# Kernel optimization log

Hardware: AMD Instinct MI355X
Metric: run time of the kernel (lower is better)

The kernel has to match this reference:

```python
import jax, jax.numpy as jnp
import numpy as np

IN_F = 4096
OUT_F = 11008
P8 = 128
P6 = 256
P4 = IN_F - P8 - P6  # 3712


def setup_inputs() -> dict:
    key = jax.random.key(0)
    k1, k2, k3, k4 = jax.random.split(key, 4)
    x = jax.random.normal(k1, (32, 8, IN_F), dtype=jnp.float32)
    W = jax.random.normal(k2, (OUT_F, IN_F), dtype=jnp.float32) * 0.02
    bias = jax.random.normal(k3, (OUT_F,), dtype=jnp.float32) * 0.01
    # channel permutation: first P4 channels -> 4-bit, next P6 -> 6-bit, last P8 -> 8-bit outliers
    reorder_index = jax.random.permutation(k4, IN_F).astype(jnp.int32)
    return {"x": x, "W": W, "bias": bias, "reorder_index": reorder_index}


def _quant(v, bits):
    # symmetric per-row quantization (per-token for acts, per-out-channel for weights)
    qmax = float(2 ** (bits - 1) - 1)
    s = jnp.max(jnp.abs(v), axis=-1, keepdims=True) / qmax
    s = jnp.where(s == 0, jnp.ones_like(s), s)
    q = jnp.round(jnp.clip(v / s, -qmax, qmax))
    return q, s


def reference(x, W, bias, reorder_index):
    bsz, q_len, F = x.shape
    xr = x.reshape(bsz * q_len, F)[:, reorder_index]  # reorder_quantize_x gather
    Wr = W[:, reorder_index]                          # reorder_quantize_w4 gather
    y = jnp.zeros((bsz * q_len, W.shape[0]), dtype=x.dtype)
    start = 0
    for bits, n in ((4, P4), (6, P6), (8, P8)):
        qa, sa = _quant(xr[:, start:start + n], bits)      # [T,n], [T,1]
        qb, sb = _quant(Wr[:, start:start + n], bits)      # [O,n], [O,1]
        # dequantized partial matmul: (qa @ qb.T) * sa * sb.T
        y = y + jnp.einsum('tn,on->to', qa, qb) * (sa * sb.T)
        start += n
    y = y + bias
    return y.reshape(bsz, q_len, -1)
```

## Files before the change

### kernel.cpp

```cpp
#include <hip/hip_runtime.h>
#include <stdint.h>

#define T_ROWS 256
#define KF 4096
#define OF 11008

typedef int   v4i __attribute__((ext_vector_type(4)));
typedef float v4f __attribute__((ext_vector_type(4)));

typedef const __attribute__((address_space(1))) uint8_t* gptr_t;
typedef __attribute__((address_space(3))) uint8_t* lptr_t;

__global__ __launch_bounds__(256) void perm_k(const int* __restrict__ idx,
                                              int* __restrict__ src_of) {
    __shared__ uint8_t g[KF];
    __shared__ int cnt[3][256];
    const int t = threadIdx.x;
    for (int i = 0; i < 16; ++i) {
        int p = t * 16 + i;
        int seg = p < 3712 ? 0 : (p < 3968 ? 1 : 2);
        g[idx[p]] = (uint8_t)seg;
    }
    __syncthreads();
    int c0 = 0, c1 = 0, c2 = 0;
    for (int i = 0; i < 16; ++i) {
        int s = g[t * 16 + i];
        c0 += (s == 0); c1 += (s == 1); c2 += (s == 2);
    }
    cnt[0][t] = c0; cnt[1][t] = c1; cnt[2][t] = c2;
    __syncthreads();
    if (t < 3) {
        int run = 0;
        for (int i = 0; i < 256; ++i) { int v = cnt[t][i]; cnt[t][i] = run; run += v; }
    }
    __syncthreads();
    int off0 = cnt[0][t], off1 = 3712 + cnt[1][t], off2 = 3968 + cnt[2][t];
    for (int i = 0; i < 16; ++i) {
        int c = t * 16 + i;
        int s = g[c];
        int d = (s == 0) ? off0++ : (s == 1) ? off1++ : off2++;
        src_of[d] = c;
    }
}

__global__ __launch_bounds__(256) void quant_k(const float* __restrict__ x,
                                               const float* __restrict__ W,
                                               const int* __restrict__ src_of,
                                               int8_t* __restrict__ qX,
                                               int8_t* __restrict__ qW,
                                               float* __restrict__ sX,
                                               float* __restrict__ sW) {
    __shared__ float rowbuf[KF];
    __shared__ float lmax[256];
    __shared__ float sm[3];
    const int b = blockIdx.x;
    const int t = threadIdx.x;
    const float* src; int8_t* qout; float* scales; int r; int nrows;
    if (b < T_ROWS) { src = x; qout = qX; scales = sX; r = b; nrows = T_ROWS; }
    else           { src = W; qout = qW; scales = sW; r = b - T_ROWS; nrows = OF; }
    const float* row = src + (size_t)r * KF;

#pragma unroll
    for (int i = 0; i < 4; ++i) {
        v4f v = *(const v4f*)(row + i * 1024 + t * 4);
        *(v4f*)&rowbuf[i * 1024 + t * 4] = v;
    }

    const int seg = t < 232 ? 0 : (t < 248 ? 1 : 2);
    const float qmax = seg == 0 ? 7.f : (seg == 1 ? 31.f : 127.f);
    int c[16];
#pragma unroll
    for (int i = 0; i < 4; ++i) {
        v4i ci = *(const v4i*)&src_of[t * 16 + i * 4];
        c[i*4+0] = ci[0]; c[i*4+1] = ci[1]; c[i*4+2] = ci[2]; c[i*4+3] = ci[3];
    }
    __syncthreads();

    float v[16];
    float mx = 0.f;
#pragma unroll
    for (int i = 0; i < 16; ++i) { v[i] = rowbuf[c[i]]; mx = fmaxf(mx, fabsf(v[i])); }
    lmax[t] = mx;
    __syncthreads();
    const int wv = t >> 6, ln = t & 63;
    if (wv == 0) {
        float m = fmaxf(fmaxf(lmax[ln], lmax[ln + 64]), lmax[ln + 128]);
        if (ln < 40) m = fmaxf(m, lmax[ln + 192]);
#pragma unroll
        for (int off = 32; off; off >>= 1) m = fmaxf(m, __shfl_xor(m, off));
        if (ln == 0) sm[0] = m;
    } else if (wv == 1) {
        float m = ln < 16 ? lmax[232 + ln] : 0.f;
#pragma unroll
        for (int off = 8; off; off >>= 1) m = fmaxf(m, __shfl_xor(m, off));
        if (ln == 0) sm[1] = m;
    } else if (wv == 2) {
        float m = ln < 8 ? lmax[248 + ln] : 0.f;
#pragma unroll
        for (int off = 4; off; off >>= 1) m = fmaxf(m, __shfl_xor(m, off));
        if (ln == 0) sm[2] = m;
    }
    __syncthreads();
    float s = sm[seg] / qmax;
    if (s == 0.f) s = 1.f;
    if (t == 0 || t == 232 || t == 248) scales[seg * nrows + r] = s;
    union { int8_t bb[16]; v4i q; } u;
#pragma unroll
    for (int i = 0; i < 16; ++i) {
        float qv = rintf(fminf(fmaxf(v[i] / s, -qmax), qmax));
        u.bb[i] = (int8_t)qv;
    }
    *(v4i*)(qout + (size_t)r * KF + t * 16) = u.q;
}

__global__ __launch_bounds__(256, 2)
void gemm_k(const int8_t* __restrict__ qX, const int8_t* __restrict__ qW,
            const float* __restrict__ sX, const float* __restrict__ sW,
            const float* __restrict__ bias, float* __restrict__ out) {
    __shared__ __align__(16) int8_t lA[3][128 * 128];
    __shared__ __align__(16) int8_t lB[3][64 * 128];

    const int bid = blockIdx.x;
    const int swz = (bid & 7) * 43 + (bid >> 3);
    const int mb = swz & 1;
    const int nb = swz >> 1;
    const int row0 = mb * 128;
    const int col0 = nb * 64;
    const int tid = threadIdx.x;
    const int lane = tid & 63;
    const int w = tid >> 6;
    const int lr = lane >> 3;
    const int lc = lane & 7;

    v4i iacc[2][4];
    v4f facc[2][4];
#pragma unroll
    for (int m = 0; m < 2; ++m)
#pragma unroll
        for (int n = 0; n < 4; ++n) {
            iacc[m][n][0]=0; iacc[m][n][1]=0; iacc[m][n][2]=0; iacc[m][n][3]=0;
            facc[m][n][0]=0.f; facc[m][n][1]=0.f; facc[m][n][2]=0.f; facc[m][n][3]=0.f;
        }

    auto stage = [&](int bf, int kstep) {
        const int k0 = kstep * 128;
        const int sc = (lc ^ lr) << 4;
#pragma unroll
        for (int j = 0; j < 4; ++j) {
            const int row = j * 32 + w * 8;
            const uint8_t* src = (const uint8_t*)qX + (size_t)(row0 + row + lr) * KF + k0 + sc;
            __builtin_amdgcn_global_load_lds((gptr_t)src, (lptr_t)&lA[bf][row * 128], 16, 0, 0);
        }
#pragma unroll
        for (int j = 0; j < 2; ++j) {
            const int row = j * 32 + w * 8;
            const uint8_t* src = (const uint8_t*)qW + (size_t)(col0 + row + lr) * KF + k0 + sc;
            __builtin_amdgcn_global_load_lds((gptr_t)src, (lptr_t)&lB[bf][row * 128], 16, 0, 0);
        }
    };

    auto flush = [&](int seg) {
#pragma unroll
        for (int m = 0; m < 2; ++m) {
            float sa[4];
#pragma unroll
            for (int rr = 0; rr < 4; ++rr)
                sa[rr] = sX[seg * T_ROWS + row0 + w * 32 + m * 16 + ((lane >> 4) << 2) + rr];
#pragma unroll
            for (int n = 0; n < 4; ++n) {
                const float sb = sW[seg * OF + col0 + n * 16 + (lane & 15)];
#pragma unroll
                for (int rr = 0; rr < 4; ++rr) {
                    facc[m][n][rr] += (float)iacc[m][n][rr] * (sa[rr] * sb);
                    iacc[m][n][rr] = 0;
                }
            }
        }
    };

    stage(0, 0);
    stage(1, 1);
    asm volatile("s_waitcnt vmcnt(6)" ::: "memory");
    __builtin_amdgcn_s_barrier();

    int cur = 0;
    for (int t = 0; t < 32; ++t) {
        if (t < 30) stage((t + 2) % 3, t + 2);
        v4i a[2][2], b2[4][2];
        const int kg = lane >> 4;
#pragma unroll
        for (int m = 0; m < 2; ++m) {
            const int row = w * 32 + m * 16 + (lane & 15);
#pragma unroll
            for (int kk = 0; kk < 2; ++kk) {
                const int ch = (kk * 4 + kg) ^ (row & 7);
                a[m][kk] = *(const v4i*)&lA[cur][row * 128 + ch * 16];
            }
        }
#pragma unroll
        for (int n = 0; n < 4; ++n) {
            const int row = n * 16 + (lane & 15);
#pragma unroll
            for (int kk = 0; kk < 2; ++kk) {
                const int ch = (kk * 4 + kg) ^ (row & 7);
                b2[n][kk] = *(const v4i*)&lB[cur][row * 128 + ch * 16];
            }
        }
        asm volatile("s_waitcnt lgkmcnt(0)" ::: "memory");
        __builtin_amdgcn_sched_barrier(0);
#pragma unroll
        for (int kk = 0; kk < 2; ++kk)
#pragma unroll
            for (int m = 0; m < 2; ++m)
#pragma unroll
                for (int n = 0; n < 4; ++n)
                    iacc[m][n] = __builtin_amdgcn_mfma_i32_16x16x64_i8(a[m][kk], b2[n][kk], iacc[m][n], 0, 0, 0);
        if (t == 28) flush(0);
        else if (t == 30) flush(1);
        if (t < 30) {
            asm volatile("s_waitcnt vmcnt(6)" ::: "memory");
            __builtin_amdgcn_s_barrier();
        } else if (t == 30) {
            asm volatile("s_waitcnt vmcnt(0)" ::: "memory");
            __builtin_amdgcn_s_barrier();
        }
        cur = (cur == 2) ? 0 : cur + 1;
    }
    flush(2);

#pragma unroll
    for (int m = 0; m < 2; ++m)
#pragma unroll
        for (int n = 0; n < 4; ++n) {
            const int colg = col0 + n * 16 + (lane & 15);
            const float bv = bias[colg];
#pragma unroll
            for (int rr = 0; rr < 4; ++rr) {
                const int rowg = row0 + w * 32 + m * 16 + ((lane >> 4) << 2) + rr;
                out[(size_t)rowg * OF + colg] = facc[m][n][rr] + bv;
            }
        }
}

extern "C" void kernel_launch(void* const* d_in, const int* in_sizes, int n_in,
                              void* d_out, int out_size, void* d_ws, size_t ws_size,
                              hipStream_t stream) {
    const float* x    = (const float*)d_in[0];
    const float* W    = (const float*)d_in[1];
    const float* bias = (const float*)d_in[2];
    const int*   ridx = (const int*)d_in[3];
    float* out = (float*)d_out;

    uint8_t* ws = (uint8_t*)d_ws;
    int8_t* qX = (int8_t*)ws;
    int8_t* qW = (int8_t*)(ws + 1048576);
    float*  sX = (float*)(ws + 46137344);
    float*  sW = (float*)(ws + 46140416);
    int* src_of = (int*)(ws + 46272512);

    perm_k<<<1, 256, 0, stream>>>(ridx, src_of);
    quant_k<<<T_ROWS + OF, 256, 0, stream>>>(x, W, src_of, qX, qW, sX, sW);
    gemm_k<<<344, 256, 0, stream>>>(qX, qW, sX, sW, bias, out);
}
```

Baseline: 79.34 us.

## Pack 4-bit weight segment as offset nibbles to cut GEMM weight traffic

Measured after the change: 83.28 us. 1.05x slower.

```diff
diff --git a/kernel.cpp b/kernel.cpp
--- a/kernel.cpp
+++ b/kernel.cpp
@@ -4,9 +4,11 @@
 #define T_ROWS 256
 #define KF 4096
 #define OF 11008
+#define WROW 2240
 
 typedef int   v4i __attribute__((ext_vector_type(4)));
 typedef float v4f __attribute__((ext_vector_type(4)));
+typedef unsigned int u32;
 
 typedef const __attribute__((address_space(1))) uint8_t* gptr_t;
 typedef __attribute__((address_space(3))) uint8_t* lptr_t;
@@ -15,6 +17,7 @@
                                               int* __restrict__ src_of) {
     __shared__ uint8_t g[KF];
     __shared__ int cnt[3][256];
+    __shared__ int exc[3][256];
     const int t = threadIdx.x;
     for (int i = 0; i < 16; ++i) {
         int p = t * 16 + i;
@@ -29,12 +32,23 @@
     }
     cnt[0][t] = c0; cnt[1][t] = c1; cnt[2][t] = c2;
     __syncthreads();
-    if (t < 3) {
+    if (t < 192) {
+        int s = t >> 6, l = t & 63;
         int run = 0;
-        for (int i = 0; i < 256; ++i) { int v = cnt[t][i]; cnt[t][i] = run; run += v; }
-    }
-    __syncthreads();
-    int off0 = cnt[0][t], off1 = 3712 + cnt[1][t], off2 = 3968 + cnt[2][t];
+        for (int j = 0; j < 4; ++j) {
+            int x = cnt[s][j * 64 + l];
+            int inc = x;
+#pragma unroll
+            for (int off = 1; off < 64; off <<= 1) {
+                int y = __shfl_up(inc, off);
+                if (l >= off) inc += y;
+            }
+            exc[s][j * 64 + l] = run + inc - x;
+            run += __shfl(inc, 63);
+        }
+    }
+    __syncthreads();
+    int off0 = exc[0][t], off1 = 3712 + exc[1][t], off2 = 3968 + exc[2][t];
     for (int i = 0; i < 16; ++i) {
         int c = t * 16 + i;
         int s = g[c];
@@ -47,23 +61,25 @@
                                                const float* __restrict__ W,
                                                const int* __restrict__ src_of,
                                                int8_t* __restrict__ qX,
-                                               int8_t* __restrict__ qW,
+                                               uint8_t* __restrict__ qWp,
                                                float* __restrict__ sX,
-                                               float* __restrict__ sW) {
+                                               float* __restrict__ sW,
+                                               int* __restrict__ S0X) {
     __shared__ float rowbuf[KF];
     __shared__ float lmax[256];
     __shared__ float sm[3];
+    __shared__ int isum[256];
     const int b = blockIdx.x;
     const int t = threadIdx.x;
-    const float* src; int8_t* qout; float* scales; int r; int nrows;
-    if (b < T_ROWS) { src = x; qout = qX; scales = sX; r = b; nrows = T_ROWS; }
-    else           { src = W; qout = qW; scales = sW; r = b - T_ROWS; nrows = OF; }
-    const float* row = src + (size_t)r * KF;
-
-#pragma unroll
-    for (int i = 0; i < 4; ++i) {
-        v4f v = *(const v4f*)(row + i * 1024 + t * 4);
-        *(v4f*)&rowbuf[i * 1024 + t * 4] = v;
+    const int w = t >> 6, lane = t & 63;
+    const bool isX = b < T_ROWS;
+    const int r = isX ? b : b - T_ROWS;
+    const float* row = (isX ? x : W) + (size_t)r * KF;
+
+#pragma unroll
+    for (int j = 0; j < 4; ++j) {
+        const uint8_t* src = (const uint8_t*)(row + j * 1024 + t * 4);
+        __builtin_amdgcn_global_load_lds((gptr_t)src, (lptr_t)&rowbuf[j * 1024 + w * 256], 16, 0, 0);
     }
 
     const int seg = t < 232 ? 0 : (t < 248 ? 1 : 2);
@@ -82,43 +98,76 @@
     for (int i = 0; i < 16; ++i) { v[i] = rowbuf[c[i]]; mx = fmaxf(mx, fabsf(v[i])); }
     lmax[t] = mx;
     __syncthreads();
-    const int wv = t >> 6, ln = t & 63;
-    if (wv == 0) {
-        float m = fmaxf(fmaxf(lmax[ln], lmax[ln + 64]), lmax[ln + 128]);
-        if (ln < 40) m = fmaxf(m, lmax[ln + 192]);
+    if (w == 0) {
+        float m = fmaxf(fmaxf(lmax[lane], lmax[lane + 64]), lmax[lane + 128]);
+        if (lane < 40) m = fmaxf(m, lmax[lane + 192]);
 #pragma unroll
         for (int off = 32; off; off >>= 1) m = fmaxf(m, __shfl_xor(m, off));
-        if (ln == 0) sm[0] = m;
-    } else if (wv == 1) {
-        float m = ln < 16 ? lmax[232 + ln] : 0.f;
+        if (lane == 0) sm[0] = m;
+    } else if (w == 1) {
+        float m = lane < 16 ? lmax[232 + lane] : 0.f;
 #pragma unroll
         for (int off = 8; off; off >>= 1) m = fmaxf(m, __shfl_xor(m, off));
-        if (ln == 0) sm[1] = m;
-    } else if (wv == 2) {
-        float m = ln < 8 ? lmax[248 + ln] : 0.f;
+        if (lane == 0) sm[1] = m;
+    } else if (w == 2) {
+        float m = lane < 8 ? lmax[248 + lane] : 0.f;
 #pragma unroll
         for (int off = 4; off; off >>= 1) m = fmaxf(m, __shfl_xor(m, off));
-        if (ln == 0) sm[2] = m;
+        if (lane == 0) sm[2] = m;
     }
     __syncthreads();
     float s = sm[seg] / qmax;
     if (s == 0.f) s = 1.f;
-    if (t == 0 || t == 232 || t == 248) scales[seg * nrows + r] = s;
-    union { int8_t bb[16]; v4i q; } u;
-#pragma unroll
-    for (int i = 0; i < 16; ++i) {
-        float qv = rintf(fminf(fmaxf(v[i] / s, -qmax), qmax));
-        u.bb[i] = (int8_t)qv;
-    }
-    *(v4i*)(qout + (size_t)r * KF + t * 16) = u.q;
+    if (t == 0 || t == 232 || t == 248)
+        (isX ? sX : sW)[seg * (isX ? T_ROWS : OF) + r] = s;
+
+    int q[16];
+#pragma unroll
+    for (int i = 0; i < 16; ++i)
+        q[i] = (int)rintf(fminf(fmaxf(v[i] / s, -qmax), qmax));
+
+    if (isX) {
+        int ss = 0;
+        union { int8_t bb[16]; v4i vv; } u;
+#pragma unroll
+        for (int i = 0; i < 16; ++i) { u.bb[i] = (int8_t)q[i]; ss += q[i]; }
+        isum[t] = (seg == 0) ? ss : 0;
+        *(v4i*)(qX + (size_t)r * KF + t * 16) = u.vv;
+        __syncthreads();
+        if (w == 0) {
+            int v2 = isum[lane] + isum[lane + 64] + isum[lane + 128] + isum[lane + 192];
+#pragma unroll
+            for (int off = 32; off; off >>= 1) v2 += __shfl_xor(v2, off);
+            if (lane == 0) S0X[r] = v2;
+        }
+    } else {
+        uint8_t* wrow = qWp + (size_t)r * WROW;
+        if (seg == 0) {
+            u32 pk[2] = {0, 0};
+#pragma unroll
+            for (int j = 0; j < 8; ++j) {
+                u32 byte = (u32)(q[2*j] + 8) | ((u32)(q[2*j+1] + 8) << 4);
+                pk[j >> 2] |= byte << ((j & 3) * 8);
+            }
+            *(u32*)(wrow + t * 8) = pk[0];
+            *(u32*)(wrow + t * 8 + 4) = pk[1];
+        } else {
+            union { int8_t bb[16]; v4i vv; } u;
+#pragma unroll
+            for (int i = 0; i < 16; ++i) u.bb[i] = (int8_t)q[i];
+            const int off = (seg == 1) ? 1856 + (t - 232) * 16 : 2112 + (t - 248) * 16;
+            *(v4i*)(wrow + off) = u.vv;
+        }
+    }
 }
 
 __global__ __launch_bounds__(256, 2)
-void gemm_k(const int8_t* __restrict__ qX, const int8_t* __restrict__ qW,
+void gemm_k(const int8_t* __restrict__ qX, const uint8_t* __restrict__ qWp,
             const float* __restrict__ sX, const float* __restrict__ sW,
+            const int* __restrict__ S0X,
             const float* __restrict__ bias, float* __restrict__ out) {
     __shared__ __align__(16) int8_t lA[3][128 * 128];
-    __shared__ __align__(16) int8_t lB[3][64 * 128];
+    __shared__ __align__(16) int8_t lB[2][64 * 128];
 
     const int bid = blockIdx.x;
     const int swz = (bid & 7) * 43 + (bid >> 3);
@@ -129,8 +178,9 @@
     const int tid = threadIdx.x;
     const int lane = tid & 63;
     const int w = tid >> 6;
-    const int lr = lane >> 3;
-    const int lc = lane & 7;
+    const int lr = lane >> 3, lc = lane & 7;
+    const int brow = tid >> 2;
+    const int bch  = tid & 3;
 
     v4i iacc[2][4];
     v4f facc[2][4];
@@ -142,59 +192,86 @@
             facc[m][n][0]=0.f; facc[m][n][1]=0.f; facc[m][n][2]=0.f; facc[m][n][3]=0.f;
         }
 
-    auto stage = [&](int bf, int kstep) {
-        const int k0 = kstep * 128;
+    auto stageA = [&](int slot, int step) {
+        const int k0 = step * 128;
         const int sc = (lc ^ lr) << 4;
 #pragma unroll
         for (int j = 0; j < 4; ++j) {
             const int row = j * 32 + w * 8;
             const uint8_t* src = (const uint8_t*)qX + (size_t)(row0 + row + lr) * KF + k0 + sc;
-            __builtin_amdgcn_global_load_lds((gptr_t)src, (lptr_t)&lA[bf][row * 128], 16, 0, 0);
-        }
-#pragma unroll
-        for (int j = 0; j < 2; ++j) {
-            const int row = j * 32 + w * 8;
-            const uint8_t* src = (const uint8_t*)qW + (size_t)(col0 + row + lr) * KF + k0 + sc;
-            __builtin_amdgcn_global_load_lds((gptr_t)src, (lptr_t)&lB[bf][row * 128], 16, 0, 0);
-        }
+            __builtin_amdgcn_global_load_lds((gptr_t)src, (lptr_t)&lA[slot][row * 128], 16, 0, 0);
+        }
+    };
+
+    auto loadB = [&](v4i (&rs)[2], int step) {
+        const uint8_t* rb = qWp + (size_t)(col0 + brow) * WROW;
+        if (step <= 28) {
+            rs[0] = *(const v4i*)(rb + step * 64 + bch * 16);
+        } else {
+            const int off = step * 128 - 1856;
+            rs[0] = *(const v4i*)(rb + off + bch * 32);
+            rs[1] = *(const v4i*)(rb + off + bch * 32 + 16);
+        }
+    };
+
+    auto writeB = [&](v4i (&rs)[2], int step) {
+        int8_t* dst = &lB[step & 1][0];
+        const int swr = brow & 7;
+        v4i w0, w1;
+        if (step <= 28) {
+#pragma unroll
+            for (int qq = 0; qq < 4; ++qq) {
+                u32 wd = ((u32)((const int*)&rs[0])[qq]);
+                u32 lo = wd & 0x0F0F0F0Fu;
+                u32 hi = (wd >> 4) & 0x0F0F0F0Fu;
+                u32 e0 = __builtin_amdgcn_perm(hi, lo, 0x05010400u);
+                u32 e1 = __builtin_amdgcn_perm(hi, lo, 0x07030602u);
+                if (qq < 2) { w0[2*qq] = (int)e0; w0[2*qq+1] = (int)e1; }
+                else        { w1[2*(qq-2)] = (int)e0; w1[2*(qq-2)+1] = (int)e1; }
+            }
+        } else {
+            w0 = rs[0]; w1 = rs[1];
+        }
+        *(v4i*)(dst + brow * 128 + ((2 * bch)     ^ swr) * 16) = w0;
+        *(v4i*)(dst + brow * 128 + ((2 * bch + 1) ^ swr) * 16) = w1;
     };
 
     auto flush = [&](int seg) {
 #pragma unroll
         for (int m = 0; m < 2; ++m) {
-            float sa[4];
-#pragma unroll
-            for (int rr = 0; rr < 4; ++rr)
-                sa[rr] = sX[seg * T_ROWS + row0 + w * 32 + m * 16 + ((lane >> 4) << 2) + rr];
+            float sa[4]; int s0[4];
+#pragma unroll
+            for (int rr = 0; rr < 4; ++rr) {
+                const int rg = row0 + w * 32 + m * 16 + ((lane >> 4) << 2) + rr;
+                sa[rr] = sX[seg * T_ROWS + rg];
+                s0[rr] = (seg == 0) ? S0X[rg] : 0;
+            }
 #pragma unroll
             for (int n = 0; n < 4; ++n) {
                 const float sb = sW[seg * OF + col0 + n * 16 + (lane & 15)];
 #pragma unroll
                 for (int rr = 0; rr < 4; ++rr) {
-                    facc[m][n][rr] += (float)iacc[m][n][rr] * (sa[rr] * sb);
+                    const int v = iacc[m][n][rr] - 8 * s0[rr];
+                    facc[m][n][rr] += (float)v * (sa[rr] * sb);
                     iacc[m][n][rr] = 0;
                 }
             }
         }
     };
 
-    stage(0, 0);
-    stage(1, 1);
-    asm volatile("s_waitcnt vmcnt(6)" ::: "memory");
-    __builtin_amdgcn_s_barrier();
-
-    int cur = 0;
-    for (int t = 0; t < 32; ++t) {
-        if (t < 30) stage((t + 2) % 3, t + 2);
-        v4i a[2][2], b2[4][2];
+    auto body = [&](int t, v4i (&rsLoad)[2], v4i (&rsWrite)[2]) {
+        __builtin_amdgcn_s_barrier();
+        v4i a[2][2], bfr[4][2];
         const int kg = lane >> 4;
+        const int8_t* pa = &lA[t % 3][0];
+        const int8_t* pb = &lB[t & 1][0];
 #pragma unroll
         for (int m = 0; m < 2; ++m) {
             const int row = w * 32 + m * 16 + (lane & 15);
 #pragma unroll
             for (int kk = 0; kk < 2; ++kk) {
                 const int ch = (kk * 4 + kg) ^ (row & 7);
-                a[m][kk] = *(const v4i*)&lA[cur][row * 128 + ch * 16];
+                a[m][kk] = *(const v4i*)(pa + row * 128 + ch * 16);
             }
         }
 #pragma unroll
@@ -203,7 +280,7 @@
 #pragma unroll
             for (int kk = 0; kk < 2; ++kk) {
                 const int ch = (kk * 4 + kg) ^ (row & 7);
-                b2[n][kk] = *(const v4i*)&lB[cur][row * 128 + ch * 16];
+                bfr[n][kk] = *(const v4i*)(pb + row * 128 + ch * 16);
             }
         }
         asm volatile("s_waitcnt lgkmcnt(0)" ::: "memory");
@@ -214,17 +291,35 @@
             for (int m = 0; m < 2; ++m)
 #pragma unroll
                 for (int n = 0; n < 4; ++n)
-                    iacc[m][n] = __builtin_amdgcn_mfma_i32_16x16x64_i8(a[m][kk], b2[n][kk], iacc[m][n], 0, 0, 0);
+                    iacc[m][n] = __builtin_amdgcn_mfma_i32_16x16x64_i8(a[m][kk], bfr[n][kk], iacc[m][n], 0, 0, 0);
         if (t == 28) flush(0);
         else if (t == 30) flush(1);
-        if (t < 30) {
-            asm volatile("s_waitcnt vmcnt(6)" ::: "memory");
-            __builtin_amdgcn_s_barrier();
-        } else if (t == 30) {
+        if (t + 2 < 32) {
+            stageA((t + 2) % 3, t + 2);
+            loadB(rsLoad, t + 2);
+            if (t + 2 <= 28) asm volatile("s_waitcnt vmcnt(5)" ::: "memory");
+            else             asm volatile("s_waitcnt vmcnt(6)" ::: "memory");
+        } else {
             asm volatile("s_waitcnt vmcnt(0)" ::: "memory");
-            __builtin_amdgcn_s_barrier();
-        }
-        cur = (cur == 2) ? 0 : cur + 1;
+        }
+        if (t + 1 < 32) {
+            writeB(rsWrite, t + 1);
+            asm volatile("s_waitcnt lgkmcnt(0)" ::: "memory");
+        }
+    };
+
+    v4i rsA_[2], rsB_[2];
+    stageA(0, 0);
+    loadB(rsA_, 0);
+    asm volatile("s_waitcnt vmcnt(0)" ::: "memory");
+    writeB(rsA_, 0);
+    stageA(1, 1);
+    loadB(rsB_, 1);
+    asm volatile("s_waitcnt lgkmcnt(0)" ::: "memory");
+
+    for (int tt = 0; tt < 32; tt += 2) {
+        body(tt,     rsA_, rsB_);
+        body(tt + 1, rsB_, rsA_);
     }
     flush(2);
 
@@ -252,13 +347,14 @@
     float* out = (float*)d_out;
 
     uint8_t* ws = (uint8_t*)d_ws;
-    int8_t* qX = (int8_t*)ws;
-    int8_t* qW = (int8_t*)(ws + 1048576);
-    float*  sX = (float*)(ws + 46137344);
-    float*  sW = (float*)(ws + 46140416);
-    int* src_of = (int*)(ws + 46272512);
+    int8_t*  qX  = (int8_t*)ws;
+    uint8_t* qWp = ws + 1048576;
+    float*   sX  = (float*)(ws + 25706496);
+    float*   sW  = (float*)(ws + 25709568);
+    int* src_of  = (int*)(ws + 25841664);
+    int* S0X     = (int*)(ws + 25858048);
 
     perm_k<<<1, 256, 0, stream>>>(ridx, src_of);
-    quant_k<<<T_ROWS + OF, 256, 0, stream>>>(x, W, src_of, qX, qW, sX, sW);
-    gemm_k<<<344, 256, 0, stream>>>(qX, qW, sX, sW, bias, out);
+    quant_k<<<T_ROWS + OF, 256, 0, stream>>>(x, W, src_of, qX, qWp, sX, sW, S0X);
+    gemm_k<<<344, 256, 0, stream>>>(qX, qWp, sX, sW, S0X, bias, out);
 }
```

## Load A operands directly to registers and parallelize permutation prefix scan

Applied to the files above, without the earlier changes.

Result: no change. 79.76 us (+0.5%).

```diff
diff --git a/kernel.cpp b/kernel.cpp
--- a/kernel.cpp
+++ b/kernel.cpp
@@ -15,6 +15,7 @@
                                               int* __restrict__ src_of) {
     __shared__ uint8_t g[KF];
     __shared__ int cnt[3][256];
+    __shared__ int exc[3][256];
     const int t = threadIdx.x;
     for (int i = 0; i < 16; ++i) {
         int p = t * 16 + i;
@@ -29,12 +30,23 @@
     }
     cnt[0][t] = c0; cnt[1][t] = c1; cnt[2][t] = c2;
     __syncthreads();
-    if (t < 3) {
+    if (t < 192) {
+        int s = t >> 6, l = t & 63;
         int run = 0;
-        for (int i = 0; i < 256; ++i) { int v = cnt[t][i]; cnt[t][i] = run; run += v; }
-    }
-    __syncthreads();
-    int off0 = cnt[0][t], off1 = 3712 + cnt[1][t], off2 = 3968 + cnt[2][t];
+        for (int j = 0; j < 4; ++j) {
+            int x = cnt[s][j * 64 + l];
+            int inc = x;
+#pragma unroll
+            for (int off = 1; off < 64; off <<= 1) {
+                int y = __shfl_up(inc, off);
+                if (l >= off) inc += y;
+            }
+            exc[s][j * 64 + l] = run + inc - x;
+            run += __shfl(inc, 63);
+        }
+    }
+    __syncthreads();
+    int off0 = exc[0][t], off1 = 3712 + exc[1][t], off2 = 3968 + exc[2][t];
     for (int i = 0; i < 16; ++i) {
         int c = t * 16 + i;
         int s = g[c];
@@ -117,20 +129,18 @@
 void gemm_k(const int8_t* __restrict__ qX, const int8_t* __restrict__ qW,
             const float* __restrict__ sX, const float* __restrict__ sW,
             const float* __restrict__ bias, float* __restrict__ out) {
-    __shared__ __align__(16) int8_t lA[3][128 * 128];
     __shared__ __align__(16) int8_t lB[3][64 * 128];
 
     const int bid = blockIdx.x;
     const int swz = (bid & 7) * 43 + (bid >> 3);
-    const int mb = swz & 1;
-    const int nb = swz >> 1;
-    const int row0 = mb * 128;
-    const int col0 = nb * 64;
+    const int row0 = (swz & 1) * 128;
+    const int col0 = (swz >> 1) * 64;
     const int tid = threadIdx.x;
     const int lane = tid & 63;
     const int w = tid >> 6;
-    const int lr = lane >> 3;
-    const int lc = lane & 7;
+    const int lr = lane >> 3, lc = lane & 7;
+    const int kg = lane >> 4;
+    const int cr = lane & 15;
 
     v4i iacc[2][4];
     v4f facc[2][4];
@@ -142,21 +152,31 @@
             facc[m][n][0]=0.f; facc[m][n][1]=0.f; facc[m][n][2]=0.f; facc[m][n][3]=0.f;
         }
 
-    auto stage = [&](int bf, int kstep) {
-        const int k0 = kstep * 128;
+    const int8_t* aRow[2];
+    aRow[0] = qX + (size_t)(row0 + w * 32 + cr) * KF;
+    aRow[1] = qX + (size_t)(row0 + w * 32 + 16 + cr) * KF;
+
+    auto stageB = [&](int slot, int step) {
+        const int k0 = step * 128;
         const int sc = (lc ^ lr) << 4;
 #pragma unroll
-        for (int j = 0; j < 4; ++j) {
-            const int row = j * 32 + w * 8;
-            const uint8_t* src = (const uint8_t*)qX + (size_t)(row0 + row + lr) * KF + k0 + sc;
-            __builtin_amdgcn_global_load_lds((gptr_t)src, (lptr_t)&lA[bf][row * 128], 16, 0, 0);
-        }
-#pragma unroll
         for (int j = 0; j < 2; ++j) {
-            const int row = j * 32 + w * 8;
-            const uint8_t* src = (const uint8_t*)qW + (size_t)(col0 + row + lr) * KF + k0 + sc;
-            __builtin_amdgcn_global_load_lds((gptr_t)src, (lptr_t)&lB[bf][row * 128], 16, 0, 0);
-        }
+            const int brow = j * 32 + w * 8;
+            const uint8_t* src = (const uint8_t*)qW + (size_t)(col0 + brow + lr) * KF + k0 + sc;
+            __builtin_amdgcn_global_load_lds((gptr_t)src, (lptr_t)&lB[slot][brow * 128], 16, 0, 0);
+        }
+    };
+
+    auto loadA = [&](v4i (&a)[2][2], int step) {
+        const int kb = step * 128 + kg * 16;
+#pragma unroll
+        for (int m = 0; m < 2; ++m)
+#pragma unroll
+            for (int kk = 0; kk < 2; ++kk) {
+                const int8_t* p = aRow[m] + kb + kk * 64;
+                asm volatile("global_load_dwordx4 %0, %1, off"
+                             : "=v"(a[m][kk]) : "v"(p) : "memory");
+            }
     };
 
     auto flush = [&](int seg) {
@@ -178,35 +198,24 @@
         }
     };
 
-    stage(0, 0);
-    stage(1, 1);
-    asm volatile("s_waitcnt vmcnt(6)" ::: "memory");
-    __builtin_amdgcn_s_barrier();
-
-    int cur = 0;
-    for (int t = 0; t < 32; ++t) {
-        if (t < 30) stage((t + 2) % 3, t + 2);
-        v4i a[2][2], b2[4][2];
-        const int kg = lane >> 4;
-#pragma unroll
-        for (int m = 0; m < 2; ++m) {
-            const int row = w * 32 + m * 16 + (lane & 15);
+    auto body = [&](int t, v4i (&aCur)[2][2], v4i (&aNext)[2][2]) {
+        __builtin_amdgcn_s_barrier();
+        v4i bf[4][2];
+        const int8_t* pb = &lB[t % 3][0];
+#pragma unroll
+        for (int n = 0; n < 4; ++n) {
+            const int brow = n * 16 + cr;
 #pragma unroll
             for (int kk = 0; kk < 2; ++kk) {
-                const int ch = (kk * 4 + kg) ^ (row & 7);
-                a[m][kk] = *(const v4i*)&lA[cur][row * 128 + ch * 16];
-            }
-        }
-#pragma unroll
-        for (int n = 0; n < 4; ++n) {
-            const int row = n * 16 + (lane & 15);
-#pragma unroll
-            for (int kk = 0; kk < 2; ++kk) {
-                const int ch = (kk * 4 + kg) ^ (row & 7);
-                b2[n][kk] = *(const v4i*)&lB[cur][row * 128 + ch * 16];
-            }
-        }
-        asm volatile("s_waitcnt lgkmcnt(0)" ::: "memory");
+                const int ch = (kk * 4 + kg) ^ (brow & 7);
+                bf[n][kk] = *(const v4i*)(pb + brow * 128 + ch * 16);
+            }
+        }
+        if (t + 2 < 32) stageB((t + 2) % 3, t + 2);
+        if (t + 1 < 32) loadA(aNext, t + 1);
+        if (t < 30)       asm volatile("s_waitcnt vmcnt(6) lgkmcnt(0)" ::: "memory");
+        else if (t == 30) asm volatile("s_waitcnt vmcnt(4) lgkmcnt(0)" ::: "memory");
+        else              asm volatile("s_waitcnt vmcnt(0) lgkmcnt(0)" ::: "memory");
         __builtin_amdgcn_sched_barrier(0);
 #pragma unroll
         for (int kk = 0; kk < 2; ++kk)
@@ -214,17 +223,20 @@
             for (int m = 0; m < 2; ++m)
 #pragma unroll
                 for (int n = 0; n < 4; ++n)
-                    iacc[m][n] = __builtin_amdgcn_mfma_i32_16x16x64_i8(a[m][kk], b2[n][kk], iacc[m][n], 0, 0, 0);
+                    iacc[m][n] = __builtin_amdgcn_mfma_i32_16x16x64_i8(aCur[m][kk], bf[n][kk], iacc[m][n], 0, 0, 0);
         if (t == 28) flush(0);
         else if (t == 30) flush(1);
-        if (t < 30) {
-            asm volatile("s_waitcnt vmcnt(6)" ::: "memory");
-            __builtin_amdgcn_s_barrier();
-        } else if (t == 30) {
-            asm volatile("s_waitcnt vmcnt(0)" ::: "memory");
-            __builtin_amdgcn_s_barrier();
-        }
-        cur = (cur == 2) ? 0 : cur + 1;
+    };
+
+    v4i aA[2][2], aB[2][2];
+    stageB(0, 0);
+    stageB(1, 1);
+    loadA(aA, 0);
+    asm volatile("s_waitcnt vmcnt(6)" ::: "memory");
+
+    for (int tt = 0; tt < 32; tt += 2) {
+        body(tt,     aA, aB);
+        body(tt + 1, aB, aA);
     }
     flush(2);
 
```
